# Performance work log

Measured on AMD Instinct MI355X. Metric: run time of the kernel, lower is better.

## Reference

```python
import jax, jax.numpy as jnp
import numpy as np

B, N, F_IN, T, K, F_OUT = 16, 1536, 64, 12, 3, 64


def setup_inputs() -> dict:
    key = jax.random.key(0)
    k1, k2, k3, k4 = jax.random.split(key, 4)
    x = jax.random.normal(k1, (B, N, F_IN, T), dtype=jnp.float32)
    spatial_attention = jax.random.uniform(k2, (B, N, N), dtype=jnp.float32)
    # stacked Chebyshev polynomials T_0..T_{K-1}, each (N, N); scaled like
    # normalized-Laplacian polynomials to keep magnitudes sane
    cheb = jax.random.normal(k3, (K, N, N), dtype=jnp.float32) * (1.0 / np.sqrt(N))
    # Theta initialized with torch.rand -> uniform[0,1)
    Theta = jax.random.uniform(k4, (K, F_IN, F_OUT), dtype=jnp.float32)
    return {"x": x, "spatial_attention": spatial_attention, "cheb": cheb, "Theta": Theta}


def reference(x, spatial_attention, cheb, Theta):
    # x: (B, N, F_in, T); spatial_attention: (B, N, N)
    # cheb: (K, N, N); Theta: (K, F_in, F_out)
    # Original per (t, k): ((T_k * At)^T @ x[..., t]) @ Theta_k, summed over k, relu.
    # Vectorized over all timesteps at once; small fixed K loop avoids a
    # (K, B, N, N) intermediate.
    n_cheb = cheb.shape[0]
    acc = jnp.zeros(x.shape[:2] + (Theta.shape[-1], x.shape[-1]), dtype=x.dtype)  # (B,N,F_out,T)
    for k in range(n_cheb):
        t_k_with_at = cheb[k][None, :, :] * spatial_attention          # (B, N, N)
        # transpose over node dims is folded into the einsum: sum over source node n
        rhs = jnp.einsum("bnm,bnft->bmft", t_k_with_at, x)             # (B, N, F_in, T)
        acc = acc + jnp.einsum("bmft,fo->bmot", rhs, Theta[k])         # (B, N, F_out, T)
    return jax.nn.relu(acc)
```

## Files before the change

### kernel.cpp

```cpp
#include <hip/hip_runtime.h>
#include <hip/hip_bf16.h>
#include <stdint.h>


#define B_    16
#define N_    1536
#define FIN_  64
#define T_    12
#define K_    3
#define FOUT_ 64
#define C_    768
#define NN_ ((size_t)N_ * N_)
#define CN_ ((size_t)C_ * N_)

typedef float          f32x4 __attribute__((ext_vector_type(4)));
typedef short          s16x8 __attribute__((ext_vector_type(8)));
typedef unsigned short u16x4 __attribute__((ext_vector_type(4)));

__device__ __forceinline__ unsigned short f2bf(float f) {
    unsigned int u = __builtin_bit_cast(unsigned int, f);
    return (unsigned short)((u + 0x8000u) >> 16);
}

__device__ __forceinline__ void gload_lds16(const void* g, void* l) {
    __builtin_amdgcn_global_load_lds(
        (const __attribute__((address_space(1))) unsigned*)g,
        (__attribute__((address_space(3))) unsigned*)l, 16, 0, 0);
}

__global__ __launch_bounds__(256) void s1_theta(const float* __restrict__ x,
                                                const float* __restrict__ Theta,
                                                unsigned short* __restrict__ Y) {
    __shared__ __align__(16) float xt[16][772];

    int bid = blockIdx.x;
    int nc = bid % 96, b = bid / 96;
    int n0 = nc * 16;
    int tid = threadIdx.x;

    const float* xg = x + (size_t)(b * N_ + n0) * 768;
#pragma unroll
    for (int i = 0; i < 12; ++i) {
        int c = i * 256 + tid;
        int row = c / 192, col = (c % 192) * 4;
        *(f32x4*)&xt[row][col] = *(const f32x4*)(xg + (size_t)c * 4);
    }
    __syncthreads();

    int oo = tid >> 4, nn = tid & 15;
    unsigned short* yp = Y + (size_t)b * (K_ * CN_) + n0 + nn;

    for (int k = 0; k < 3; ++k) {
        const float* th = Theta + (size_t)k * 4096 + oo * 4;
        float acc[4][12];
#pragma unroll
        for (int j = 0; j < 4; ++j)
#pragma unroll
            for (int t = 0; t < 12; ++t) acc[j][t] = 0.f;

        for (int f = 0; f < 64; ++f) {
            f32x4 xv0 = *(const f32x4*)&xt[nn][f * 12];
            f32x4 xv1 = *(const f32x4*)&xt[nn][f * 12 + 4];
            f32x4 xv2 = *(const f32x4*)&xt[nn][f * 12 + 8];
            f32x4 tv  = *(const f32x4*)(th + (size_t)f * 64);
#pragma unroll
            for (int j = 0; j < 4; ++j) {
#pragma unroll
                for (int t = 0; t < 4; ++t) {
                    acc[j][t]     += tv[j] * xv0[t];
                    acc[j][t + 4] += tv[j] * xv1[t];
                    acc[j][t + 8] += tv[j] * xv2[t];
                }
            }
        }
#pragma unroll
        for (int j = 0; j < 4; ++j)
#pragma unroll
            for (int t = 0; t < 12; ++t) {
                int c = (oo * 4 + j) * 12 + t;
                yp[((size_t)k * C_ + c) * N_] = f2bf(acc[j][t]);
            }
    }
}

__global__ __launch_bounds__(256, 3) void s2_gemm(const float* __restrict__ At,
                                                  const float* __restrict__ cheb,
                                                  const unsigned short* __restrict__ Y,
                                                  float* __restrict__ out) {
    __shared__ __align__(16) unsigned short Alds[2][128 * 40];
    __shared__ __align__(16) unsigned short Blds[2][128 * 32];

    int hb = blockIdx.x;
    int lb = (hb & 7) * 144 + (hb >> 3);
    int mt = lb % 12;
    int ct = (lb / 12) % 6;
    int b  = lb / 72;
    int m0 = mt * 128, c0 = ct * 128;

    int tid  = threadIdx.x;
    int lane = tid & 63, wave = tid >> 6;
    int wr = (wave >> 1) * 64, wc = (wave & 1) * 64;
    int l15 = lane & 15;

    int q = tid & 7, g = tid >> 3;

    const float* cb = cheb + (size_t)(q * 4) * N_ + (m0 + g * 4);
    const float* ab = At + (size_t)b * NN_ + (size_t)(q * 4) * N_ + (m0 + g * 4);

    int lrow = lane >> 2;
    int lchunk = (lane & 3) ^ (lrow & 3);
    const unsigned short* yb = Y + (size_t)(b * K_) * CN_
                               + (size_t)(c0 + wave * 16 + lrow) * N_ + lchunk * 8;

    int awb = g * 320 + q * 8;
    int ard = (wr + l15) * 80 + (lane >> 4) * 16;
    int brd = (wc + l15) * 64 + (((lane >> 4) ^ (lane & 3)) << 4);

    f32x4 acc[4][4];
#pragma unroll
    for (int mi = 0; mi < 4; ++mi)
#pragma unroll
        for (int ci = 0; ci < 4; ++ci) acc[mi][ci] = (f32x4)0.f;

    f32x4 cv[4], av[4];

#define PFREG(DNT, KC) do {                                                  \
    const float* cbk_ = cb + (size_t)(KC) * NN_ + (size_t)(DNT) * 32 * N_;   \
    const float* abk_ = ab + (size_t)(DNT) * 32 * N_;                        \
    _Pragma("unroll") for (int j = 0; j < 4; ++j) {                          \
        cv[j] = *(const f32x4*)(cbk_ + (size_t)j * N_);                      \
        av[j] = *(const f32x4*)(abk_ + (size_t)j * N_); } } while (0)

#define YDMA(PN, DNT, KC) do {                                               \
    const unsigned short* ys_ = yb + (size_t)(KC) * CN_ + (DNT) * 32;        \
    char* bl_ = (char*)Blds[PN] + wave * 1024;                               \
    gload_lds16(ys_, bl_);                                                   \
    gload_lds16(ys_ + (size_t)64 * N_, bl_ + 4096); } while (0)

#define WBUILD(PN) do {                                                      \
    f32x4 w_[4];                                                             \
    _Pragma("unroll") for (int j = 0; j < 4; ++j) w_[j] = cv[j] * av[j];     \
    _Pragma("unroll") for (int i = 0; i < 4; ++i) {                          \
        u16x4 pk_ = { f2bf(w_[0][i]), f2bf(w_[1][i]),                        \
                      f2bf(w_[2][i]), f2bf(w_[3][i]) };                      \
        *(u16x4*)((char*)Alds[PN] + awb + i * 80) = pk_; } } while (0)

#define STEP(P, DNTn, KCn, DNTnn, KCnn, DOSTAGE, DOLOAD) do {                \
    if (DOSTAGE) { YDMA((P) ^ 1, DNTn, KCn); WBUILD((P) ^ 1); }              \
    if (DOLOAD)  { PFREG(DNTnn, KCnn); }                                     \
    const char* Ab_ = (const char*)Alds[P];                                  \
    const char* Bb_ = (const char*)Blds[P];                                  \
    s16x8 af_[4], bv_[4];                                                    \
    _Pragma("unroll") for (int mi = 0; mi < 4; ++mi)                         \
        af_[mi] = *(const s16x8*)(Ab_ + ard + mi * 1280);                    \
    _Pragma("unroll") for (int ci = 0; ci < 4; ++ci)                         \
        bv_[ci] = *(const s16x8*)(Bb_ + brd + ci * 1024);                    \
    _Pragma("unroll") for (int mi = 0; mi < 4; ++mi)                         \
        _Pragma("unroll") for (int ci = 0; ci < 4; ++ci)                     \
            acc[mi][ci] = __builtin_amdgcn_mfma_f32_16x16x32_bf16(           \
                af_[mi], bv_[ci], acc[mi][ci], 0, 0, 0);                     \
    __syncthreads(); } while (0)

    PFREG(0, 0);
    YDMA(0, 0, 0);
    WBUILD(0);
    PFREG(0, 1);
    __syncthreads();

    for (int it2 = 0; it2 < 24; ++it2) {
        bool more = (it2 != 23);
        STEP(0, 0, 1, 0, 2, true, true);
        STEP(1, 0, 2, 1, 0, true, true);
        STEP(0, 1, 0, 1, 1, true, true);
        STEP(1, 1, 1, 1, 2, true, true);
        STEP(0, 1, 2, 2, 0, true, more);
        STEP(1, 2, 0, 2, 1, more, more);
        cb += (size_t)64 * N_;
        ab += (size_t)64 * N_;
        yb += 64;
    }
#undef PFREG
#undef YDMA
#undef WBUILD
#undef STEP

    int rbase = (lane >> 4) * 4;
#pragma unroll
    for (int mi = 0; mi < 4; ++mi) {
#pragma unroll
        for (int ci = 0; ci < 4; ++ci) {
            int m = m0 + wr + mi * 16 + rbase;
            int c = c0 + wc + ci * 16 + l15;
            float* op = out + (size_t)(b * N_ + m) * C_ + c;
#pragma unroll
            for (int r = 0; r < 4; ++r) {
                float v = acc[mi][ci][r];
                op[(size_t)r * C_] = v > 0.f ? v : 0.f;
            }
        }
    }
}

extern "C" void kernel_launch(void* const* d_in, const int* in_sizes, int n_in,
                              void* d_out, int out_size, void* d_ws, size_t ws_size,
                              hipStream_t stream) {
    const float* x    = (const float*)d_in[0];
    const float* At   = (const float*)d_in[1];
    const float* cheb = (const float*)d_in[2];
    const float* Th   = (const float*)d_in[3];
    unsigned short* Y = (unsigned short*)d_ws;
    float* out = (float*)d_out;

    s1_theta<<<dim3(B_ * 96),     dim3(256), 0, stream>>>(x, Th, Y);
    s2_gemm <<<dim3(B_ * 12 * 6), dim3(256), 0, stream>>>(At, cheb, Y, out);
}
```

Baseline: 1.003 ms.

## Deepen s2_gemm prefetch pipeline with explicit vmcnt waits and Theta LDS staging

```diff
diff --git a/kernel.cpp b/kernel.cpp
--- a/kernel.cpp
+++ b/kernel.cpp
@@ -5,10 +5,8 @@
 
 #define B_    16
 #define N_    1536
-#define FIN_  64
 #define T_    12
 #define K_    3
-#define FOUT_ 64
 #define C_    768
 #define NN_ ((size_t)N_ * N_)
 #define CN_ ((size_t)C_ * N_)
@@ -28,10 +26,17 @@
         (__attribute__((address_space(3))) unsigned*)l, 16, 0, 0);
 }
 
+#define VMWAIT_(N) asm volatile("s_waitcnt vmcnt(" #N ")" ::: "memory")
+#define VMWAIT(N)  VMWAIT_(N)
+#define LGKM0      asm volatile("s_waitcnt lgkmcnt(0)" ::: "memory")
+#define SBAR       __builtin_amdgcn_s_barrier()
+#define SCHED0     __builtin_amdgcn_sched_barrier(0)
+
 __global__ __launch_bounds__(256) void s1_theta(const float* __restrict__ x,
                                                 const float* __restrict__ Theta,
                                                 unsigned short* __restrict__ Y) {
     __shared__ __align__(16) float xt[16][772];
+    __shared__ __align__(16) float tht[4096];
 
     int bid = blockIdx.x;
     int nc = bid % 96, b = bid / 96;
@@ -45,13 +50,16 @@
         int row = c / 192, col = (c % 192) * 4;
         *(f32x4*)&xt[row][col] = *(const f32x4*)(xg + (size_t)c * 4);
     }
+#pragma unroll
+    for (int i = 0; i < 4; ++i)
+        *(f32x4*)&tht[i * 1024 + tid * 4] =
+            *(const f32x4*)(Theta + i * 1024 + tid * 4);
     __syncthreads();
 
     int oo = tid >> 4, nn = tid & 15;
     unsigned short* yp = Y + (size_t)b * (K_ * CN_) + n0 + nn;
 
     for (int k = 0; k < 3; ++k) {
-        const float* th = Theta + (size_t)k * 4096 + oo * 4;
         float acc[4][12];
 #pragma unroll
         for (int j = 0; j < 4; ++j)
@@ -62,7 +70,7 @@
             f32x4 xv0 = *(const f32x4*)&xt[nn][f * 12];
             f32x4 xv1 = *(const f32x4*)&xt[nn][f * 12 + 4];
             f32x4 xv2 = *(const f32x4*)&xt[nn][f * 12 + 8];
-            f32x4 tv  = *(const f32x4*)(th + (size_t)f * 64);
+            f32x4 tv  = *(const f32x4*)&tht[f * 64 + oo * 4];
 #pragma unroll
             for (int j = 0; j < 4; ++j) {
 #pragma unroll
@@ -80,6 +88,14 @@
                 int c = (oo * 4 + j) * 12 + t;
                 yp[((size_t)k * C_ + c) * N_] = f2bf(acc[j][t]);
             }
+        if (k < 2) {
+            __syncthreads();
+#pragma unroll
+            for (int i = 0; i < 4; ++i)
+                *(f32x4*)&tht[i * 1024 + tid * 4] =
+                    *(const f32x4*)(Theta + (size_t)(k + 1) * 4096 + i * 1024 + tid * 4);
+            __syncthreads();
+        }
     }
 }
 
@@ -122,14 +138,18 @@
 #pragma unroll
         for (int ci = 0; ci < 4; ++ci) acc[mi][ci] = (f32x4)0.f;
 
-    f32x4 cv[4], av[4];
-
-#define PFREG(DNT, KC) do {                                                  \
-    const float* cbk_ = cb + (size_t)(KC) * NN_ + (size_t)(DNT) * 32 * N_;   \
-    const float* abk_ = ab + (size_t)(DNT) * 32 * N_;                        \
-    _Pragma("unroll") for (int j = 0; j < 4; ++j) {                          \
-        cv[j] = *(const f32x4*)(cbk_ + (size_t)j * N_);                      \
-        av[j] = *(const f32x4*)(abk_ + (size_t)j * N_); } } while (0)
+    f32x4 cv[4];
+    f32x4 av0[4], av1[4];
+
+#define PFCV(DNT, KC) do {                                                   \
+    const float* p_ = cb + (size_t)(KC) * NN_ + (size_t)(DNT) * 32 * N_;     \
+    _Pragma("unroll") for (int j = 0; j < 4; ++j)                            \
+        cv[j] = *(const f32x4*)(p_ + (size_t)j * N_); } while (0)
+
+#define PFAV(AV, DNT) do {                                                   \
+    const float* p_ = ab + (size_t)(DNT) * 32 * N_;                          \
+    _Pragma("unroll") for (int j = 0; j < 4; ++j)                            \
+        AV[j] = *(const f32x4*)(p_ + (size_t)j * N_); } while (0)
 
 #define YDMA(PN, DNT, KC) do {                                               \
     const unsigned short* ys_ = yb + (size_t)(KC) * CN_ + (DNT) * 32;        \
@@ -137,17 +157,24 @@
     gload_lds16(ys_, bl_);                                                   \
     gload_lds16(ys_ + (size_t)64 * N_, bl_ + 4096); } while (0)
 
-#define WBUILD(PN) do {                                                      \
+#define WBUILD(PN, AV) do {                                                  \
     f32x4 w_[4];                                                             \
-    _Pragma("unroll") for (int j = 0; j < 4; ++j) w_[j] = cv[j] * av[j];     \
+    _Pragma("unroll") for (int j = 0; j < 4; ++j) w_[j] = cv[j] * AV[j];     \
     _Pragma("unroll") for (int i = 0; i < 4; ++i) {                          \
         u16x4 pk_ = { f2bf(w_[0][i]), f2bf(w_[1][i]),                        \
                       f2bf(w_[2][i]), f2bf(w_[3][i]) };                      \
         *(u16x4*)((char*)Alds[PN] + awb + i * 80) = pk_; } } while (0)
 
-#define STEP(P, DNTn, KCn, DNTnn, KCnn, DOSTAGE, DOLOAD) do {                \
-    if (DOSTAGE) { YDMA((P) ^ 1, DNTn, KCn); WBUILD((P) ^ 1); }              \
-    if (DOLOAD)  { PFREG(DNTnn, KCnn); }                                     \
+#define STEP(P, AVC, AVL, SD,SK, CD,CK, AD, NWAIT, DOS, DOCV, DOAV) do {     \
+    if (DOS)  { YDMA((P)^1, SD, SK); WBUILD((P)^1, AVC); }                   \
+    if (DOCV) { PFCV(CD, CK); }                                              \
+    if (DOAV) { PFAV(AVL, AD); }                                             \
+    SCHED0;                                                                  \
+    LGKM0;                                                                   \
+    VMWAIT(NWAIT);                                                           \
+    SCHED0;                                                                  \
+    SBAR;                                                                    \
+    SCHED0;                                                                  \
     const char* Ab_ = (const char*)Alds[P];                                  \
     const char* Bb_ = (const char*)Blds[P];                                  \
     s16x8 af_[4], bv_[4];                                                    \
@@ -159,27 +186,47 @@
         _Pragma("unroll") for (int ci = 0; ci < 4; ++ci)                     \
             acc[mi][ci] = __builtin_amdgcn_mfma_f32_16x16x32_bf16(           \
                 af_[mi], bv_[ci], acc[mi][ci], 0, 0, 0);                     \
-    __syncthreads(); } while (0)
-
-    PFREG(0, 0);
+    SCHED0;                                                                  \
+    SBAR;                                                                    \
+    SCHED0;                                                                  \
+} while (0)
+
+    PFAV(av0, 0);
+    PFCV(0, 0);
+    WBUILD(0, av0);
+    PFAV(av1, 0);
+    PFAV(av0, 0);
+    PFCV(0, 1);
     YDMA(0, 0, 0);
-    WBUILD(0);
-    PFREG(0, 1);
-    __syncthreads();
-
-    for (int it2 = 0; it2 < 24; ++it2) {
-        bool more = (it2 != 23);
-        STEP(0, 0, 1, 0, 2, true, true);
-        STEP(1, 0, 2, 1, 0, true, true);
-        STEP(0, 1, 0, 1, 1, true, true);
-        STEP(1, 1, 1, 1, 2, true, true);
-        STEP(0, 1, 2, 2, 0, true, more);
-        STEP(1, 2, 0, 2, 1, more, more);
-        cb += (size_t)64 * N_;
-        ab += (size_t)64 * N_;
-        yb += 64;
-    }
-#undef PFREG
+
+    STEP(0, av1, av1, 0,1, 0,2, 1, 18, 1,1,1);
+    STEP(1, av0, av0, 0,2, 1,0, 1, 34, 1,1,1);
+    STEP(0, av1, av1, 1,0, 1,1, 1, 34, 1,1,1);
+    STEP(1, av0, av0, 1,1, 1,2, 2, 34, 1,1,1);
+    STEP(0, av1, av1, 1,2, 2,0, 2, 34, 1,1,1);
+    STEP(1, av0, av0, 2,0, 2,1, 2, 34, 1,1,1);
+    cb += (size_t)64 * N_;  ab += (size_t)64 * N_;  yb += 64;
+
+#pragma unroll 1
+    for (int it2 = 1; it2 < 23; ++it2) {
+        STEP(0, av1, av1, 0,1, 0,2, 1, 34, 1,1,1);
+        STEP(1, av0, av0, 0,2, 1,0, 1, 34, 1,1,1);
+        STEP(0, av1, av1, 1,0, 1,1, 1, 34, 1,1,1);
+        STEP(1, av0, av0, 1,1, 1,2, 2, 34, 1,1,1);
+        STEP(0, av1, av1, 1,2, 2,0, 2, 34, 1,1,1);
+        STEP(1, av0, av0, 2,0, 2,1, 2, 34, 1,1,1);
+        cb += (size_t)64 * N_;  ab += (size_t)64 * N_;  yb += 64;
+    }
+
+    STEP(0, av1, av1, 0,1, 0,2, 1, 34, 1,1,1);
+    STEP(1, av0, av0, 0,2, 1,0, 1, 34, 1,1,1);
+    STEP(0, av1, av1, 1,0, 1,1, 1, 34, 1,1,1);
+    STEP(1, av0, av0, 1,1, 1,2, 0, 26, 1,1,0);
+    STEP(0, av1, av1, 1,2, 0,0, 0, 10, 1,0,0);
+    STEP(1, av0, av0, 0,0, 0,0, 0,  0, 0,0,0);
+
+#undef PFCV
+#undef PFAV
 #undef YDMA
 #undef WBUILD
 #undef STEP
```

New measurement: 1.142 ms. 13.9% more time.
